# Optimization experiments

Hardware: AMD Instinct MI355X
Metric: run time of the kernel (lower is better)

Reference implementation:

```python
import jax, jax.numpy as jnp
import numpy as np

EPS = 1e-7        # Hyperboloid.eps for float32
MIN_NORM = 1e-15
MAX_NORM = 1e6
K = 1.0           # c = 1 -> K = 1/c
SQRT_K = 1.0
SLOPE = 0.01      # nn.LeakyReLU default negative_slope


def _cosh(x):
    return jnp.cosh(jnp.clip(x, -15.0, 15.0))


def _sinh(x):
    return jnp.sinh(jnp.clip(x, -15.0, 15.0))


def _arcosh(x):
    x = jnp.clip(x, 1.0 + 1e-7)
    return jnp.log(x + jnp.sqrt(x * x - 1.0))


def _norm(y):
    # safe row-norm (grad-finite at 0); original clamps norm to >=1e-15 anyway
    return jnp.sqrt(jnp.clip(jnp.sum(y * y, axis=-1, keepdims=True), 1e-30))


def mdot(x, y):
    return jnp.sum(x * y, axis=-1, keepdims=True) - 2.0 * x[..., :1] * y[..., :1]


def mnorm(u):
    return jnp.sqrt(jnp.clip(mdot(u, u), EPS))


def proj(x):
    y = x[..., 1:]
    x0 = jnp.sqrt(jnp.clip(K + jnp.sum(y * y, axis=-1, keepdims=True), EPS))
    return jnp.concatenate([x0, y], axis=-1)


def proj_tan0(u):
    return jnp.concatenate([jnp.zeros_like(u[..., :1]), u[..., 1:]], axis=-1)


def proj_tan(u, x):
    ux = jnp.sum(x[..., 1:] * u[..., 1:], axis=-1, keepdims=True)
    v0 = ux / jnp.clip(x[..., :1], EPS)
    return jnp.concatenate([v0, u[..., 1:]], axis=-1)


def expmap0(u):
    y = u[..., 1:]
    yn = jnp.clip(_norm(y), MIN_NORM)
    theta = yn / SQRT_K
    r0 = SQRT_K * _cosh(theta)
    r = SQRT_K * _sinh(theta) * y / yn
    return proj(jnp.concatenate([r0, r], axis=-1))


def logmap0(x):
    y = x[..., 1:]
    yn = jnp.clip(_norm(y), MIN_NORM)
    theta = jnp.clip(x[..., :1] / SQRT_K, 1.0 + EPS)
    r = SQRT_K * _arcosh(theta) * y / yn
    return jnp.concatenate([jnp.zeros_like(x[..., :1]), r], axis=-1)


def expmap(u, x):
    nu = jnp.clip(mnorm(u), None, MAX_NORM)
    theta = jnp.clip(nu / SQRT_K, MIN_NORM)
    return proj(_cosh(theta) * x + _sinh(theta) * u / theta)


def ptransp0(x, u):
    x0 = x[..., :1]
    y = x[..., 1:]
    yn = jnp.clip(_norm(y), MIN_NORM)
    y_hat = y / yn
    v = jnp.concatenate([-yn, (SQRT_K - x0) * y_hat], axis=-1)
    alpha = jnp.sum(y_hat * u[..., 1:], axis=-1, keepdims=True) / SQRT_K
    return proj_tan(u - alpha * v, x)


def mobius_add(x, y):
    u = logmap0(y)
    v = ptransp0(x, u)
    return expmap(v, x)


def hgcn_forward(x, adj, weight, bias):
    # map Euclidean input to the hyperboloid (HGCN.encode prologue)
    xh = proj(expmap0(proj_tan0(x)))
    # HypLinear: mobius_matvec (logmap0 -> matmul -> expmap0) + hyperbolic bias add
    res = proj(expmap0(logmap0(xh) @ weight.T))
    hyp_bias = proj(expmap0(proj_tan0(bias[None, :])))
    res = proj(mobius_add(res, hyp_bias))
    # HypAgg (use_att=False): aggregate in tangent space at origin via spmm
    h = proj(expmap0(adj @ logmap0(res)))
    # HypAct: LeakyReLU in tangent space, then back to hyperboloid
    t = proj_tan0(jax.nn.leaky_relu(logmap0(h), SLOPE))
    return proj(expmap0(t))


def setup_inputs() -> dict:
    key = jax.random.key(0)
    k1, k2, k3, k4 = jax.random.split(key, 4)
    N, D = 8192, 64
    x = jax.random.normal(k1, (N, D), dtype=jnp.float32)
    adj = jax.random.uniform(k2, (N, N), dtype=jnp.float32)
    adj = adj / jnp.sum(adj, axis=1, keepdims=True)  # row-normalized dense adjacency
    weight = jax.random.uniform(k3, (D, D), dtype=jnp.float32)  # init.uniform_ in [0,1)
    bias = 0.01 * jax.random.normal(k4, (D,), dtype=jnp.float32)
    return {"x": x, "adj": adj, "weight": weight, "bias": bias}


def reference(x, adj, weight, bias):
    return hgcn_forward(x, adj, weight, bias)
```

## Files before the change

kernel.cpp:

```cpp
#include <hip/hip_runtime.h>
#include <hip/hip_bf16.h>
#include <math.h>

typedef __bf16 bf16x8 __attribute__((ext_vector_type(8)));
typedef float  f32x4  __attribute__((ext_vector_type(4)));

#define NND 8192
#define DIM 64
#define PB  10368

__device__ __forceinline__ float wsum(float v) {
#pragma unroll
    for (int m = 1; m < 64; m <<= 1) v += __shfl_xor(v, m, 64);
    return v;
}

struct SC { float sh, ch; };
__device__ __forceinline__ SC sinhcosh(float c) {
    float e  = expf(c);
    float ei = 1.0f / e;
    SC r; r.sh = 0.5f * (e - ei); r.ch = 0.5f * (e + ei);
    return r;
}

__device__ __forceinline__ float arcosh_from_n2(float n2) {
    float t = fmaxf(n2, 2.0000001e-7f);
    return logf(sqrtf(1.0f + t) + sqrtf(t));
}

__device__ __forceinline__ float tangent_chain(float xv, int lane) {
    float y   = (lane == 0) ? 0.0f : xv;
    float yn2 = wsum(y * y);
    float yn  = fmaxf(sqrtf(fmaxf(yn2, 1e-30f)), 1e-15f);
    SC s1 = sinhcosh(fminf(yn, 15.0f));
    float r   = (lane == 0) ? 0.0f : s1.sh * y / yn;
    float rn2 = wsum(r * r);
    float ynb = fmaxf(sqrtf(fmaxf(rn2, 1e-30f)), 1e-15f);
    float ac  = arcosh_from_n2(rn2);
    return (lane == 0) ? 0.0f : ac * r / ynb;
}

__device__ __forceinline__ float second_chain(float m, float ubv, float theta_b, int lane) {
    float my  = (lane == 0) ? 0.0f : m;
    float mn2 = wsum(my * my);
    float mn  = fmaxf(sqrtf(fmaxf(mn2, 1e-30f)), 1e-15f);
    SC s2 = sinhcosh(fminf(mn, 15.0f));
    float rr   = (lane == 0) ? 0.0f : s2.sh * my / mn;
    float rrn2 = wsum(rr * rr);
    float res0 = sqrtf(fmaxf(1.0f + rrn2, 1e-7f));
    float yn3   = fmaxf(sqrtf(fmaxf(rrn2, 1e-30f)), 1e-15f);
    float yhat  = (lane == 0) ? 0.0f : rr / yn3;
    float alpha = wsum(yhat * ubv);
    float w_    = ubv - alpha * (1.0f - res0) * yhat;
    float ux    = wsum(rr * w_);
    float v0    = ux / fmaxf(res0, 1e-7f);
    float vv    = (lane == 0) ? v0 : w_;
    float resv  = (lane == 0) ? res0 : rr;
    float theta = theta_b;
    SC s3 = sinhcosh(fminf(theta, 15.0f));
    float pv  = s3.ch * resv + s3.sh * vv / theta;
    float pn2 = wsum((lane == 0) ? 0.0f : pv * pv);
    float yn4 = fmaxf(sqrtf(fmaxf(pn2, 1e-30f)), 1e-15f);
    float ac4 = arcosh_from_n2(pn2);
    return (lane == 0) ? 0.0f : ac4 * pv / yn4;
}

__device__ __forceinline__ float epilogue_chain(float hv, int lane) {
    float y   = (lane == 0) ? 0.0f : hv;
    float yn2 = wsum(y * y);
    float yn  = fmaxf(sqrtf(fmaxf(yn2, 1e-30f)), 1e-15f);
    SC s1 = sinhcosh(fminf(yn, 15.0f));
    float r   = (lane == 0) ? 0.0f : s1.sh * y / yn;
    float rn2 = wsum(r * r);
    float ynb = fmaxf(sqrtf(fmaxf(rn2, 1e-30f)), 1e-15f);
    float ac  = arcosh_from_n2(rn2);
    float lgv = (lane == 0) ? 0.0f : ac * r / ynb;
    float t   = (lgv > 0.0f) ? lgv : 0.01f * lgv;
    float tn2 = wsum(t * t);
    float tn  = fmaxf(sqrtf(fmaxf(tn2, 1e-30f)), 1e-15f);
    SC s3 = sinhcosh(fminf(tn, 15.0f));
    float ov  = (lane == 0) ? 0.0f : s3.sh * t / tn;
    float on2 = wsum(ov * ov);
    float o0  = sqrtf(fmaxf(1.0f + on2, 1e-7f));
    return (lane == 0) ? o0 : ov;
}

__global__ __launch_bounds__(256) void k_prep(
    const float* __restrict__ x, const float* __restrict__ weight,
    const float* __restrict__ bias, __bf16* __restrict__ l2bf)
{
    __shared__ float WL[64][65];
    const int tid  = threadIdx.x;
    const int lane = tid & 63;
    const int wave = tid >> 6;
#pragma unroll
    for (int i = 0; i < 16; ++i) {
        int idx = i * 256 + tid;
        WL[idx >> 6][idx & 63] = weight[idx];
    }
    __syncthreads();
    float ubv  = tangent_chain(bias[lane], lane);
    float nub2 = wsum(ubv * ubv);
    float thb  = fmaxf(fminf(sqrtf(fmaxf(nub2, 1e-7f)), 1e6f), 1e-15f);

    const int row = blockIdx.x * 4 + wave;
    float xv  = x[row * 64 + lane];
    float L1v = tangent_chain(xv, lane);
    float mj0 = 0.f, mj1 = 0.f, mj2 = 0.f, mj3 = 0.f;
#pragma unroll
    for (int d = 0; d < 64; d += 4) {
        mj0 = fmaf(__shfl(L1v, d,     64), WL[lane][d],     mj0);
        mj1 = fmaf(__shfl(L1v, d + 1, 64), WL[lane][d + 1], mj1);
        mj2 = fmaf(__shfl(L1v, d + 2, 64), WL[lane][d + 2], mj2);
        mj3 = fmaf(__shfl(L1v, d + 3, 64), WL[lane][d + 3], mj3);
    }
    float mj  = (mj0 + mj1) + (mj2 + mj3);
    float L2v = second_chain(mj, ubv, thb, lane);
    l2bf[(size_t)lane * PB + row] = (__bf16)L2v;
}

__global__ __launch_bounds__(256, 4) void k_mm(
    const float* __restrict__ adj, const __bf16* __restrict__ l2bf,
    float* __restrict__ pws)
{
    __shared__ float AL[2][32][132];
    const int tid  = threadIdx.x;
    const int lane = tid & 63;
    const int w    = tid >> 6;
    const int l15  = lane & 15;
    const int lg   = lane >> 4;
    const int h    = blockIdx.x & 3;
    const int rb   = blockIdx.x >> 2;
    const int R0   = rb * 32;
    const int kq   = h * 2048;

    const int srow = tid >> 5;
    const int scol = (tid & 31) * 4;

    const __bf16* bp = l2bf + (size_t)(16 * w + l15) * PB + kq + 8 * lg;

    f32x4 accL = {0.f, 0.f, 0.f, 0.f};
    f32x4 accH = accL;

    {
        const float* g = adj + (size_t)(R0 + srow) * NND + kq + scol;
        f32x4 s0 = *reinterpret_cast<const f32x4*>(g);
        f32x4 s1 = *reinterpret_cast<const f32x4*>(g + (size_t)8  * NND);
        f32x4 s2 = *reinterpret_cast<const f32x4*>(g + (size_t)16 * NND);
        f32x4 s3 = *reinterpret_cast<const f32x4*>(g + (size_t)24 * NND);
        *reinterpret_cast<f32x4*>(&AL[0][srow     ][scol]) = s0;
        *reinterpret_cast<f32x4*>(&AL[0][srow +  8][scol]) = s1;
        *reinterpret_cast<f32x4*>(&AL[0][srow + 16][scol]) = s2;
        *reinterpret_cast<f32x4*>(&AL[0][srow + 24][scol]) = s3;
    }
    __syncthreads();

    for (int t = 0; t < 16; ++t) {
        const int cur = t & 1;
        f32x4 s0, s1, s2, s3;
        const bool pf = (t < 15);
        if (pf) {
            const float* g = adj + (size_t)(R0 + srow) * NND + kq + (t + 1) * 128 + scol;
            s0 = *reinterpret_cast<const f32x4*>(g);
            s1 = *reinterpret_cast<const f32x4*>(g + (size_t)8  * NND);
            s2 = *reinterpret_cast<const f32x4*>(g + (size_t)16 * NND);
            s3 = *reinterpret_cast<const f32x4*>(g + (size_t)24 * NND);
        }
#pragma unroll
        for (int ks = 0; ks < 4; ++ks) {
            const int kk = t * 128 + ks * 32;
            bf16x8 b = *reinterpret_cast<const bf16x8*>(bp + kk);
            const float* arL = &AL[cur][l15     ][ks * 32 + 8 * lg];
            const float* arH = &AL[cur][16 + l15][ks * 32 + 8 * lg];
            f32x4 a0 = *reinterpret_cast<const f32x4*>(arL);
            f32x4 a1 = *reinterpret_cast<const f32x4*>(arL + 4);
            f32x4 c0 = *reinterpret_cast<const f32x4*>(arH);
            f32x4 c1 = *reinterpret_cast<const f32x4*>(arH + 4);
            bf16x8 avL, avH;
            avL[0] = (__bf16)a0[0]; avL[1] = (__bf16)a0[1];
            avL[2] = (__bf16)a0[2]; avL[3] = (__bf16)a0[3];
            avL[4] = (__bf16)a1[0]; avL[5] = (__bf16)a1[1];
            avL[6] = (__bf16)a1[2]; avL[7] = (__bf16)a1[3];
            avH[0] = (__bf16)c0[0]; avH[1] = (__bf16)c0[1];
            avH[2] = (__bf16)c0[2]; avH[3] = (__bf16)c0[3];
            avH[4] = (__bf16)c1[0]; avH[5] = (__bf16)c1[1];
            avH[6] = (__bf16)c1[2]; avH[7] = (__bf16)c1[3];
            accL = __builtin_amdgcn_mfma_f32_16x16x32_bf16(avL, b, accL, 0, 0, 0);
            accH = __builtin_amdgcn_mfma_f32_16x16x32_bf16(avH, b, accH, 0, 0, 0);
        }
        __syncthreads();
        if (pf) {
            *reinterpret_cast<f32x4*>(&AL[cur ^ 1][srow     ][scol]) = s0;
            *reinterpret_cast<f32x4*>(&AL[cur ^ 1][srow +  8][scol]) = s1;
            *reinterpret_cast<f32x4*>(&AL[cur ^ 1][srow + 16][scol]) = s2;
            *reinterpret_cast<f32x4*>(&AL[cur ^ 1][srow + 24][scol]) = s3;
        }
        __syncthreads();
    }

    float* pp = pws + (size_t)h * NND * DIM;
#pragma unroll
    for (int i = 0; i < 4; ++i) {
        pp[(size_t)(R0 +      lg * 4 + i) * DIM + 16 * w + l15] = accL[i];
        pp[(size_t)(R0 + 16 + lg * 4 + i) * DIM + 16 * w + l15] = accH[i];
    }
}

__global__ __launch_bounds__(256) void k_fin(
    const float* __restrict__ pws, float* __restrict__ out)
{
    const int tid  = threadIdx.x;
    const int lane = tid & 63;
    const int wave = tid >> 6;
    const int row  = blockIdx.x * 4 + wave;
    const size_t base = (size_t)row * DIM + lane;
    const size_t S = (size_t)NND * DIM;
    float hv = (pws[base] + pws[S + base]) + (pws[2 * S + base] + pws[3 * S + base]);
    out[base] = epilogue_chain(hv, lane);
}

extern "C" void kernel_launch(void* const* d_in, const int* in_sizes, int n_in,
                              void* d_out, int out_size, void* d_ws, size_t ws_size,
                              hipStream_t stream)
{
    const float* x      = (const float*)d_in[0];
    const float* adj    = (const float*)d_in[1];
    const float* weight = (const float*)d_in[2];
    const float* bias   = (const float*)d_in[3];
    float* out = (float*)d_out;
    __bf16* l2bf = (__bf16*)d_ws;
    float*  pws  = (float*)((char*)d_ws + 0x180000);

    k_prep<<<2048, 256, 0, stream>>>(x, weight, bias, l2bf);
    k_mm<<<1024, 256, 0, stream>>>(adj, l2bf, pws);
    k_fin<<<2048, 256, 0, stream>>>(pws, out);
}
```

Measured before the change: 94.81 us.

## Restructure adj matmul into 16-row strided tiles with 8-way K split and bf16 LDS

The k_mm kernel now gives each block 16 strided rows (stride 512) by a 1024-wide K window, split eight ways instead of four. All adjacency loads are issued up front, converted once to bf16 and stored in an XOR-swizzled LDS tile. The double-buffered pipelined loop and its per-iteration barriers are gone, and each wave runs a single MFMA accumulator chain. The cost is twice the partial-sum workspace traffic in k_fin, the loss of load/compute overlap inside a block, and lower occupancy from the launch bound.

```diff
diff --git a/kernel.cpp b/kernel.cpp
--- a/kernel.cpp
+++ b/kernel.cpp
@@ -3,6 +3,7 @@
 #include <math.h>
 
 typedef __bf16 bf16x8 __attribute__((ext_vector_type(8)));
+typedef __bf16 bf16x4 __attribute__((ext_vector_type(4)));
 typedef float  f32x4  __attribute__((ext_vector_type(4)));
 
 #define NND 8192
@@ -119,90 +120,54 @@
     l2bf[(size_t)lane * PB + row] = (__bf16)L2v;
 }
 
-__global__ __launch_bounds__(256, 4) void k_mm(
+__global__ __launch_bounds__(256, 2) void k_mm(
     const float* __restrict__ adj, const __bf16* __restrict__ l2bf,
     float* __restrict__ pws)
 {
-    __shared__ float AL[2][32][132];
+    __shared__ __bf16 AS[16 * 1024];
     const int tid  = threadIdx.x;
     const int lane = tid & 63;
     const int w    = tid >> 6;
     const int l15  = lane & 15;
     const int lg   = lane >> 4;
-    const int h    = blockIdx.x & 3;
-    const int rb   = blockIdx.x >> 2;
-    const int R0   = rb * 32;
-    const int kq   = h * 2048;
-
-    const int srow = tid >> 5;
-    const int scol = (tid & 31) * 4;
-
-    const __bf16* bp = l2bf + (size_t)(16 * w + l15) * PB + kq + 8 * lg;
-
-    f32x4 accL = {0.f, 0.f, 0.f, 0.f};
-    f32x4 accH = accL;
-
-    {
-        const float* g = adj + (size_t)(R0 + srow) * NND + kq + scol;
-        f32x4 s0 = *reinterpret_cast<const f32x4*>(g);
-        f32x4 s1 = *reinterpret_cast<const f32x4*>(g + (size_t)8  * NND);
-        f32x4 s2 = *reinterpret_cast<const f32x4*>(g + (size_t)16 * NND);
-        f32x4 s3 = *reinterpret_cast<const f32x4*>(g + (size_t)24 * NND);
-        *reinterpret_cast<f32x4*>(&AL[0][srow     ][scol]) = s0;
-        *reinterpret_cast<f32x4*>(&AL[0][srow +  8][scol]) = s1;
-        *reinterpret_cast<f32x4*>(&AL[0][srow + 16][scol]) = s2;
-        *reinterpret_cast<f32x4*>(&AL[0][srow + 24][scol]) = s3;
+    const int j    = blockIdx.x >> 3;
+    const int kw8  = blockIdx.x & 7;
+    const int kwin = kw8 * 1024;
+
+    f32x4 v[16];
+#pragma unroll
+    for (int i = 0; i < 16; ++i) {
+        const float* gp = adj + (size_t)(512 * i + j) * NND + kwin + tid * 4;
+        v[i] = *reinterpret_cast<const f32x4*>(gp);
+    }
+
+    const int c  = tid >> 1;
+    const int h8 = (tid & 1) * 4;
+#pragma unroll
+    for (int i = 0; i < 16; ++i) {
+        __bf16* dst = AS + i * 1024 + (c ^ (i & 7)) * 8 + h8;
+        bf16x4 pv;
+        pv[0] = (__bf16)v[i][0]; pv[1] = (__bf16)v[i][1];
+        pv[2] = (__bf16)v[i][2]; pv[3] = (__bf16)v[i][3];
+        *reinterpret_cast<bf16x4*>(dst) = pv;
     }
     __syncthreads();
 
-    for (int t = 0; t < 16; ++t) {
-        const int cur = t & 1;
-        f32x4 s0, s1, s2, s3;
-        const bool pf = (t < 15);
-        if (pf) {
-            const float* g = adj + (size_t)(R0 + srow) * NND + kq + (t + 1) * 128 + scol;
-            s0 = *reinterpret_cast<const f32x4*>(g);
-            s1 = *reinterpret_cast<const f32x4*>(g + (size_t)8  * NND);
-            s2 = *reinterpret_cast<const f32x4*>(g + (size_t)16 * NND);
-            s3 = *reinterpret_cast<const f32x4*>(g + (size_t)24 * NND);
-        }
-#pragma unroll
-        for (int ks = 0; ks < 4; ++ks) {
-            const int kk = t * 128 + ks * 32;
-            bf16x8 b = *reinterpret_cast<const bf16x8*>(bp + kk);
-            const float* arL = &AL[cur][l15     ][ks * 32 + 8 * lg];
-            const float* arH = &AL[cur][16 + l15][ks * 32 + 8 * lg];
-            f32x4 a0 = *reinterpret_cast<const f32x4*>(arL);
-            f32x4 a1 = *reinterpret_cast<const f32x4*>(arL + 4);
-            f32x4 c0 = *reinterpret_cast<const f32x4*>(arH);
-            f32x4 c1 = *reinterpret_cast<const f32x4*>(arH + 4);
-            bf16x8 avL, avH;
-            avL[0] = (__bf16)a0[0]; avL[1] = (__bf16)a0[1];
-            avL[2] = (__bf16)a0[2]; avL[3] = (__bf16)a0[3];
-            avL[4] = (__bf16)a1[0]; avL[5] = (__bf16)a1[1];
-            avL[6] = (__bf16)a1[2]; avL[7] = (__bf16)a1[3];
-            avH[0] = (__bf16)c0[0]; avH[1] = (__bf16)c0[1];
-            avH[2] = (__bf16)c0[2]; avH[3] = (__bf16)c0[3];
-            avH[4] = (__bf16)c1[0]; avH[5] = (__bf16)c1[1];
-            avH[6] = (__bf16)c1[2]; avH[7] = (__bf16)c1[3];
-            accL = __builtin_amdgcn_mfma_f32_16x16x32_bf16(avL, b, accL, 0, 0, 0);
-            accH = __builtin_amdgcn_mfma_f32_16x16x32_bf16(avH, b, accH, 0, 0, 0);
-        }
-        __syncthreads();
-        if (pf) {
-            *reinterpret_cast<f32x4*>(&AL[cur ^ 1][srow     ][scol]) = s0;
-            *reinterpret_cast<f32x4*>(&AL[cur ^ 1][srow +  8][scol]) = s1;
-            *reinterpret_cast<f32x4*>(&AL[cur ^ 1][srow + 16][scol]) = s2;
-            *reinterpret_cast<f32x4*>(&AL[cur ^ 1][srow + 24][scol]) = s3;
-        }
-        __syncthreads();
-    }
-
-    float* pp = pws + (size_t)h * NND * DIM;
+    const __bf16* bp = l2bf + (size_t)(16 * w + l15) * PB + kwin + 8 * lg;
+    f32x4 acc = {0.f, 0.f, 0.f, 0.f};
+#pragma unroll
+    for (int ks = 0; ks < 32; ++ks) {
+        const __bf16* ar = AS + l15 * 1024 + (((4 * ks + lg) ^ (l15 & 7)) * 8);
+        bf16x8 a = *reinterpret_cast<const bf16x8*>(ar);
+        bf16x8 b = *reinterpret_cast<const bf16x8*>(bp + 32 * ks);
+        acc = __builtin_amdgcn_mfma_f32_16x16x32_bf16(a, b, acc, 0, 0, 0);
+    }
+
+    float* pp = pws + (size_t)kw8 * NND * DIM;
 #pragma unroll
     for (int i = 0; i < 4; ++i) {
-        pp[(size_t)(R0 +      lg * 4 + i) * DIM + 16 * w + l15] = accL[i];
-        pp[(size_t)(R0 + 16 + lg * 4 + i) * DIM + 16 * w + l15] = accH[i];
+        const int ri = lg * 4 + i;
+        pp[(size_t)(512 * ri + j) * DIM + 16 * w + l15] = acc[i];
     }
 }
 
@@ -215,7 +180,8 @@
     const int row  = blockIdx.x * 4 + wave;
     const size_t base = (size_t)row * DIM + lane;
     const size_t S = (size_t)NND * DIM;
-    float hv = (pws[base] + pws[S + base]) + (pws[2 * S + base] + pws[3 * S + base]);
+    float hv = (((pws[base] + pws[S + base]) + (pws[2*S + base] + pws[3*S + base]))
+             +  ((pws[4*S + base] + pws[5*S + base]) + (pws[6*S + base] + pws[7*S + base])));
     out[base] = epilogue_chain(hv, lane);
 }
 
@@ -232,6 +198,6 @@
     float*  pws  = (float*)((char*)d_ws + 0x180000);
 
     k_prep<<<2048, 256, 0, stream>>>(x, weight, bias, l2bf);
-    k_mm<<<1024, 256, 0, stream>>>(adj, l2bf, pws);
+    k_mm<<<4096, 256, 0, stream>>>(adj, l2bf, pws);
     k_fin<<<2048, 256, 0, stream>>>(pws, out);
 }
```

Measured after the change: 112.6 us. 1.19x slower.
